# Performance work log

Hardware: AMD Instinct MI355X
Metric: run time of the kernel (lower is better)

Reference implementation:

```python
import jax, jax.numpy as jnp
import numpy as np

NL = 4   # numLayers (modules are shared across layers)
H = 8    # numSignalHeads; contextAttention has embed_dim=1 with 1 head


def _ln(x, g, b, eps=1e-10):
    m = x.mean(-1, keepdims=True)
    v = ((x - m) ** 2).mean(-1, keepdims=True)
    return (x - m) / jnp.sqrt(v + eps) * g + b


def _forward(signalData, contextualData, Ws, bs, bn_g, bn_b,
             cWq, cWk, cWv, cbq, cbk, cbv, cbias_k, cbias_v, cWo, cbo,
             xWq, xWk, xWv, xbq, xbk, xbv, xbias_k, xbias_v, xWo, xbo,
             W1, b1, W2, b2, W3, b3,
             ln_ff_g, ln_ff_b, ln_cas_g, ln_cas_b, ln_fin_g, ln_fin_b):
    B, S, E = signalData.shape
    dh = E // H
    scale = float(1.0 / np.sqrt(dh))
    # synthesizeContext: Linear(C,18) + BatchNorm1d(18, track_running_stats=False -> batch stats)
    ec = contextualData @ Ws.T + bs                       # (B,18)
    mu = ec.mean(0)
    var = ((ec - mu) ** 2).mean(0)                        # biased var (PyTorch BN)
    ec = (ec - mu) / jnp.sqrt(var + 1e-5) * bn_g + bn_b
    ec = ec[:, :, None]                                   # (B,18,1)
    sig = signalData
    for _ in range(NL):
        # --- self-attention on context: embed_dim=1, 1 head (head_dim=1, scale=1), add_bias_kv ---
        q = ec @ cWq.T + cbq                              # (B,18,1)
        k = jnp.concatenate([ec @ cWk.T + cbk, jnp.broadcast_to(cbias_k, (B, 1, 1))], axis=1)
        v = jnp.concatenate([ec @ cWv.T + cbv, jnp.broadcast_to(cbias_v, (B, 1, 1))], axis=1)
        a = jax.nn.softmax(jnp.einsum('bqd,bkd->bqk', q, k), axis=-1)
        sa = jnp.einsum('bqk,bkd->bqd', a, v) @ cWo.T + cbo
        ec = ec + sa
        # --- cross-attention: query/value = LN(signal) (E), key = context (kdim=1), add_bias_kv ---
        ns = _ln(sig, ln_cas_g, ln_cas_b)
        q = (ns @ xWq.T + xbq).reshape(B, S, H, dh)
        k = jnp.concatenate([ec @ xWk.T + xbk, jnp.broadcast_to(xbias_k, (B, 1, E))], axis=1).reshape(B, S + 1, H, dh)
        v = jnp.concatenate([ns @ xWv.T + xbv, jnp.broadcast_to(xbias_v, (B, 1, E))], axis=1).reshape(B, S + 1, H, dh)
        a = jax.nn.softmax(jnp.einsum('bqhd,bkhd->bhqk', q, k) * scale, axis=-1)
        ca = jnp.einsum('bhqk,bkhd->bqhd', a, v).reshape(B, S, E) @ xWo.T + xbo
        sig = sig + ca
        # --- feed-forward: Linear->SiLU->Linear->SiLU->Linear->SiLU (dropout = identity in eval) ---
        nf = _ln(sig, ln_ff_g, ln_ff_b)
        ff = jax.nn.silu(jax.nn.silu(jax.nn.silu(nf @ W1.T + b1) @ W2.T + b2) @ W3.T + b3)
        sig = sig + ff
    return _ln(sig, ln_fin_g, ln_fin_b)


def setup_inputs() -> dict:
    key = jax.random.key(0)
    ks = iter(jax.random.split(key, 48))
    r = lambda *s: jax.random.normal(next(ks), s, dtype=jnp.float32) * 0.05
    B, S, E, C = 4096, 18, 256, 512
    return dict(
        signalData=jax.random.normal(next(ks), (B, S, E), dtype=jnp.float32),
        contextualData=jax.random.normal(next(ks), (B, C), dtype=jnp.float32),
        Ws=r(18, C), bs=r(18), bn_g=jnp.ones(18, jnp.float32), bn_b=jnp.zeros(18, jnp.float32),
        cWq=r(1, 1), cWk=r(1, 1), cWv=r(1, 1), cbq=r(1), cbk=r(1), cbv=r(1),
        cbias_k=r(1), cbias_v=r(1), cWo=r(1, 1), cbo=r(1),
        xWq=r(E, E), xWk=r(E, 1), xWv=r(E, E), xbq=r(E), xbk=r(E), xbv=r(E),
        xbias_k=r(E), xbias_v=r(E), xWo=r(E, E), xbo=r(E),
        W1=r(32, E), b1=r(32), W2=r(16, 32), b2=r(16), W3=r(E, 16), b3=r(E),
        ln_ff_g=jnp.ones(E, jnp.float32), ln_ff_b=jnp.zeros(E, jnp.float32),
        ln_cas_g=jnp.ones(E, jnp.float32), ln_cas_b=jnp.zeros(E, jnp.float32),
        ln_fin_g=jnp.ones(E, jnp.float32), ln_fin_b=jnp.zeros(E, jnp.float32),
    )


def reference(signalData, contextualData, Ws, bs, bn_g, bn_b,
              cWq, cWk, cWv, cbq, cbk, cbv, cbias_k, cbias_v, cWo, cbo,
              xWq, xWk, xWv, xbq, xbk, xbv, xbias_k, xbias_v, xWo, xbo,
              W1, b1, W2, b2, W3, b3,
              ln_ff_g, ln_ff_b, ln_cas_g, ln_cas_b, ln_fin_g, ln_fin_b):
    return _forward(signalData, contextualData, Ws, bs, bn_g, bn_b,
                    cWq, cWk, cWv, cbq, cbk, cbv, cbias_k, cbias_v, cWo, cbo,
                    xWq, xWk, xWv, xbq, xbk, xbv, xbias_k, xbias_v, xWo, xbo,
                    W1, b1, W2, b2, W3, b3,
                    ln_ff_g, ln_ff_b, ln_cas_g, ln_cas_b, ln_fin_g, ln_fin_b)
```

## Files before the change

kernel.cpp:

```cpp
#include <hip/hip_runtime.h>

typedef unsigned short u16;
typedef __attribute__((ext_vector_type(8))) short bf16x8;
typedef __attribute__((ext_vector_type(4))) float f32x4;
typedef __attribute__((ext_vector_type(4))) unsigned int u32x4;
typedef __attribute__((ext_vector_type(2))) unsigned int u32x2;

#define MROWS 18
#define MT 2
#define SWZ(r,c)  ((c) ^ (((r)&7)<<3))
#define SWZV(n,j) ((j) ^ (((n)&3)<<3))
#define SWZP(i,j) ((j) ^ (((i)&3)<<3))

__device__ inline u16 f2bf(float f){
  unsigned int u = __float_as_uint(f);
  return (u16)((u + 0x7fffu + ((u>>16)&1u)) >> 16);
}
__device__ inline unsigned int packbf(float a, float b){
  return (unsigned int)f2bf(a) | ((unsigned int)f2bf(b)<<16);
}
__device__ inline float bfloat_lo(unsigned int u){ return __uint_as_float(u<<16); }
__device__ inline float bfloat_hi(unsigned int u){ return __uint_as_float(u & 0xffff0000u); }
__device__ inline float bf2f(u16 h){ return __uint_as_float(((unsigned int)h)<<16); }
__device__ inline float wred(float v){
  #pragma unroll
  for (int m=1;m<64;m<<=1) v += __shfl_xor(v, m, 64);
  return v;
}
__device__ inline float silu_f(float x){ return x / (1.f + __expf(-x)); }
__device__ inline f32x4 mfma16(bf16x8 a, bf16x8 b, f32x4 c){
  return __builtin_amdgcn_mfma_f32_16x16x32_bf16(a, b, c, 0, 0, 0);
}

struct Params {
  const float *sigIn;
  const float *bn_g, *bn_b;
  const float *cWq,*cWk,*cWv,*cbq,*cbk,*cbv,*cbias_k,*cbias_v,*cWo,*cbo;
  const float *xbv, *xbias_v, *xbo;
  const float *b1,*b2,*b3;
  const float *g_cas,*b_cas,*g_ff,*b_ff,*g_fin,*b_fin;
  const u16 *Wv,*Wo,*Wq3,*W1b,*W2b,*W3p;
  const float *bias3, *ecr_t, *mu, *rstd;
  float *out;
};

__global__ void k_prep(const float* __restrict__ xWq, const float* __restrict__ xWk,
                       const float* __restrict__ xWv, const float* __restrict__ xWo,
                       const float* __restrict__ xbq, const float* __restrict__ xbk,
                       const float* __restrict__ xbias_k,
                       const float* __restrict__ W1, const float* __restrict__ W2,
                       const float* __restrict__ W3,
                       u16* Wv, u16* Wo, u16* Wq3, u16* W1b, u16* W2b, u16* W3p, float* bias3){
  const int gid = blockIdx.x*blockDim.x + threadIdx.x;
  const int gsz = gridDim.x*blockDim.x;
  for (int i=gid;i<65536;i+=gsz) Wv[i]=f2bf(xWv[i]);
  for (int i=gid;i<65536;i+=gsz) Wo[i]=f2bf(xWo[i]);
  for (int i=gid;i<8192;i+=gsz)  W1b[i]=f2bf(W1[i]);
  for (int i=gid;i<512;i+=gsz)   W2b[i]=f2bf(W2[i]);
  for (int i=gid;i<8192;i+=gsz){ int o=i>>5, k=i&31; W3p[i] = (k<16)? f2bf(W3[o*16+k]) : (u16)0; }
  for (int i=gid;i<8192;i+=gsz){
    int r=i>>8, c=i&255;
    u16 outv = 0;
    if (r<24){
      int h=r&7, sel=r>>3;
      const float* vec = sel==0? xWk : (sel==1? xbk : xbias_k);
      float s=0.f;
      for (int d=0;d<32;++d) s += xWq[(size_t)(h*32+d)*256+c]*vec[h*32+d];
      outv = f2bf(s);
    }
    Wq3[i]=outv;
  }
  for (int i=gid;i<24;i+=gsz){
    int h=i&7, sel=i>>3;
    const float* vec = sel==0? xWk : (sel==1? xbk : xbias_k);
    float s=0.f; for (int d=0;d<32;++d) s += xbq[h*32+d]*vec[h*32+d];
    bias3[i]=s;
  }
}

__global__ void k_ec(const float* __restrict__ ctx, const float* __restrict__ Ws,
                     const float* __restrict__ bs, float* __restrict__ ecr_t){
  const int wave = threadIdx.x>>6, lane = threadIdx.x&63;
  const int b = blockIdx.x*4 + wave;
  const float* c = ctx + (size_t)b*512 + lane*8;
  const float4 a0 = *(const float4*)c, a1 = *(const float4*)(c+4);
  float cv[8] = {a0.x,a0.y,a0.z,a0.w,a1.x,a1.y,a1.z,a1.w};
  #pragma unroll 1
  for (int j=0;j<18;++j){
    const float* w = Ws + j*512 + lane*8;
    const float4 w0 = *(const float4*)w, w1 = *(const float4*)(w+4);
    float s = cv[0]*w0.x + cv[1]*w0.y + cv[2]*w0.z + cv[3]*w0.w
            + cv[4]*w1.x + cv[5]*w1.y + cv[6]*w1.z + cv[7]*w1.w;
    s = wred(s);
    if (lane==0) ecr_t[(size_t)j*4096 + b] = s + bs[j];
  }
}

__global__ void k_bn(const float* __restrict__ ecr_t, float* __restrict__ mu, float* __restrict__ rstd){
  __shared__ float red[256];
  const int j = blockIdx.x, tid = threadIdx.x;
  float s=0.f, s2=0.f;
  for (int b=tid;b<4096;b+=256){ float v = ecr_t[(size_t)j*4096+b]; s+=v; s2+=v*v; }
  red[tid]=s; __syncthreads();
  for (int o=128;o>0;o>>=1){ if(tid<o) red[tid]+=red[tid+o]; __syncthreads(); }
  float S = red[0]; __syncthreads();
  red[tid]=s2; __syncthreads();
  for (int o=128;o>0;o>>=1){ if(tid<o) red[tid]+=red[tid+o]; __syncthreads(); }
  float S2 = red[0];
  if (tid==0){ float m = S*(1.f/4096.f); float v = S2*(1.f/4096.f) - m*m;
               mu[j]=m; rstd[j]=rsqrtf(v+1e-5f); }
}

__global__ __launch_bounds__(256, 2) void k_main(Params P){
  __shared__ __attribute__((aligned(16))) u16 s_sig[MROWS][256];
  __shared__ __attribute__((aligned(16))) u16 s_ns [MROWS][256];
  __shared__ __attribute__((aligned(16))) u16 s_vT [256][32];
  __shared__ __attribute__((aligned(16))) u16 s_p  [8][MROWS][32];
  __shared__ __attribute__((aligned(16))) u16 s_h1 [MROWS][32];
  __shared__ float s_qq[MROWS][24];
  __shared__ float s_ec[MROWS];
  __shared__ float s_inv[8][MROWS];

  const int tid  = threadIdx.x;
  const int wave = tid >> 6;
  const int lane = tid & 63;
  const int lr   = lane & 15;
  const int lkg  = lane >> 4;
  const int kof  = lkg * 8;
  const int dr   = lkg * 4;
  const int b0   = blockIdx.x;

  for (int idx = tid*8; idx < MROWS*256; idx += 256*8){
    const int row = idx >> 8, col = idx & 255;
    const float* src = P.sigIn + (size_t)b0*18*256 + idx;
    const float4 a = *(const float4*)src;
    const float4 b = *(const float4*)(src+4);
    u32x4 w;
    w[0]=packbf(a.x,a.y); w[1]=packbf(a.z,a.w);
    w[2]=packbf(b.x,b.y); w[3]=packbf(b.z,b.w);
    *(u32x4*)&s_sig[row][SWZ(row,col)] = w;
  }
  {
    const int n = tid;
    s_vT[n][SWZV(n,19)] = 0;
    #pragma unroll
    for (int jp=10; jp<16; ++jp) *(unsigned int*)&s_vT[n][SWZV(n,2*jp)] = 0u;
    s_vT[n][SWZV(n,18)] = f2bf(P.xbias_v[n]);
  }
  if (lane < 36){
    const int h = 2*wave + (lane>=18 ? 1:0);
    const int i = lane - (lane>=18 ? 18:0);
    #pragma unroll
    for (int jp=10; jp<16; ++jp) *(unsigned int*)&s_p[h][i][SWZP(i,2*jp)] = 0u;
  }
  if (tid < MROWS){
    const float raw = P.ecr_t[(size_t)tid*4096 + b0];
    s_ec[tid] = (raw - P.mu[tid]) * P.rstd[tid] * P.bn_g[tid] + P.bn_b[tid];
  }
  __syncthreads();

  auto ln_rows = [&](const float* g, const float* bvec, int wbase, int wstep){
    for (int r = wbase; r < MROWS; r += wstep){
      const int col = lane*4;
      const u32x2 raw = *(const u32x2*)&s_sig[r][SWZ(r,col)];
      const float x0 = bfloat_lo(raw[0]), x1 = bfloat_hi(raw[0]);
      const float x2 = bfloat_lo(raw[1]), x3 = bfloat_hi(raw[1]);
      const float m = wred(x0+x1+x2+x3)*(1.f/256.f);
      const float d0=x0-m, d1=x1-m, d2=x2-m, d3=x3-m;
      const float rs = rsqrtf(wred(d0*d0+d1*d1+d2*d2+d3*d3)*(1.f/256.f)+1e-10f);
      const float4 gv = *(const float4*)(g+col);
      const float4 bv = *(const float4*)(bvec+col);
      u32x2 o;
      o[0] = packbf(d0*rs*gv.x+bv.x, d1*rs*gv.y+bv.y);
      o[1] = packbf(d2*rs*gv.z+bv.z, d3*rs*gv.w+bv.w);
      *(u32x2*)&s_ns[r][SWZ(r,col)] = o;
    }
  };

  for (int layer = 0; layer < 4; ++layer){
    if (wave == 0){
      if (lane < MROWS){
        const int i = lane;
        const float cwq=P.cWq[0], cbq=P.cbq[0], cwk=P.cWk[0], cbk=P.cbk[0];
        const float cwv=P.cWv[0], cbv=P.cbv[0], ck1=P.cbias_k[0], cv1=P.cbias_v[0];
        const float cwo=P.cWo[0], cbo=P.cbo[0];
        const float qi = s_ec[i]*cwq + cbq;
        float mx = qi*ck1;
        #pragma unroll
        for (int j=0;j<18;++j) mx = fmaxf(mx, qi*(s_ec[j]*cwk + cbk));
        float den=0.f, o=0.f;
        #pragma unroll
        for (int j=0;j<18;++j){
          const float pp=__expf(qi*(s_ec[j]*cwk + cbk)-mx);
          den+=pp; o+=pp*(s_ec[j]*cwv+cbv);
        }
        const float pp=__expf(qi*ck1-mx); den+=pp; o+=pp*cv1;
        s_ec[i] = s_ec[i] + (o/den)*cwo + cbo;
      }
    } else {
      ln_rows(P.g_cas, P.b_cas, wave-1, 3);
    }
    __syncthreads();

    {
      f32x4 accV[MT][4]; f32x4 accQ[MT];
      #pragma unroll
      for (int mt=0;mt<MT;++mt){
        accQ[mt] = f32x4{0.f,0.f,0.f,0.f};
        #pragma unroll
        for (int nt=0;nt<4;++nt) accV[mt][nt] = f32x4{0.f,0.f,0.f,0.f};
      }
      for (int kk=0; kk<8; ++kk){
        const int k0 = kk*32 + kof;
        bf16x8 afr[MT];
        #pragma unroll
        for (int mt=0;mt<MT;++mt){
          const int row = mt*16 + lr;
          u32x4 raw = u32x4{0u,0u,0u,0u};
          if (row < MROWS) raw = *(const u32x4*)&s_ns[row][SWZ(row,k0)];
          afr[mt] = __builtin_bit_cast(bf16x8, raw);
        }
        #pragma unroll
        for (int nt=0;nt<4;++nt){
          const int n = (wave*4+nt)*16 + lr;
          const bf16x8 bfr = __builtin_bit_cast(bf16x8, *(const u32x4*)(P.Wv + (size_t)n*256 + k0));
          #pragma unroll
          for (int mt=0;mt<MT;++mt) accV[mt][nt] = mfma16(afr[mt], bfr, accV[mt][nt]);
        }
        if (wave < 2){
          const bf16x8 bq = __builtin_bit_cast(bf16x8, *(const u32x4*)(P.Wq3 + (size_t)(wave*16+lr)*256 + k0));
          #pragma unroll
          for (int mt=0;mt<MT;++mt) accQ[mt] = mfma16(afr[mt], bq, accQ[mt]);
        }
      }
      #pragma unroll
      for (int nt=0;nt<4;++nt){
        const int n = (wave*4+nt)*16 + lr;
        const float bias = P.xbv[n];
        #pragma unroll
        for (int mt=0;mt<MT;++mt){
          const int c0 = mt*16 + dr;
          if (c0 + 3 < MROWS){
            u32x2 w;
            w[0] = packbf(accV[mt][nt][0]+bias, accV[mt][nt][1]+bias);
            w[1] = packbf(accV[mt][nt][2]+bias, accV[mt][nt][3]+bias);
            *(u32x2*)&s_vT[n][SWZV(n,c0)] = w;
          } else if (c0 < MROWS){
            #pragma unroll
            for (int q=0;q<2;++q) s_vT[n][SWZV(n,c0+q)] = f2bf(accV[mt][nt][q]+bias);
          }
        }
      }
      if (wave < 2){
        const int c = wave*16 + lr;
        if (c < 24){
          const float bias = P.bias3[c];
          #pragma unroll
          for (int mt=0;mt<MT;++mt){
            #pragma unroll
            for (int q=0;q<4;++q){
              const int row = mt*16 + dr + q;
              if (row < MROWS) s_qq[row][c] = accQ[mt][q] + bias;
            }
          }
        }
      }
    }
    __syncthreads();

    if (lane < 36){
      const int h = 2*wave + (lane>=18 ? 1:0);
      const int i = lane - (lane>=18 ? 18:0);
      const float scale = 0.17677669529663687f;
      const float qw = s_qq[i][h]*scale, qb = s_qq[i][8+h]*scale, s18 = s_qq[i][16+h]*scale;
      float mx = s18;
      #pragma unroll
      for (int j=0;j<18;++j) mx = fmaxf(mx, qw*s_ec[j] + qb);
      float den = 0.f;
      #pragma unroll
      for (int jj=0;jj<9;++jj){
        const float p0 = __expf(qw*s_ec[2*jj]   + qb - mx);
        const float p1 = __expf(qw*s_ec[2*jj+1] + qb - mx);
        den += p0 + p1;
        *(unsigned int*)&s_p[h][i][SWZP(i,2*jj)] = packbf(p0, p1);
      }
      const float p18 = __expf(s18 - mx); den += p18;
      *(unsigned int*)&s_p[h][i][SWZP(i,18)] = packbf(p18, 0.f);
      s_inv[h][i] = 1.f/den;
    }

    #pragma unroll
    for (int hb=0; hb<2; ++hb){
      const int h = wave*2 + hb;
      const bf16x8 a0 = __builtin_bit_cast(bf16x8, *(const u32x4*)&s_p[h][lr][SWZP(lr,kof)]);
      u32x4 zr = u32x4{0u,0u,0u,0u};
      if (lr < 2) zr = *(const u32x4*)&s_p[h][16+lr][SWZP(16+lr,kof)];
      const bf16x8 a1 = __builtin_bit_cast(bf16x8, zr);
      f32x4 d[MT][2];
      #pragma unroll
      for (int nt=0;nt<2;++nt){
        const int vn = h*32 + nt*16 + lr;
        const bf16x8 b = __builtin_bit_cast(bf16x8, *(const u32x4*)&s_vT[vn][SWZV(vn,kof)]);
        d[0][nt] = mfma16(a0, b, f32x4{0.f,0.f,0.f,0.f});
        d[1][nt] = mfma16(a1, b, f32x4{0.f,0.f,0.f,0.f});
      }
      #pragma unroll
      for (int nt=0;nt<2;++nt){
        #pragma unroll
        for (int mt=0;mt<MT;++mt){
          #pragma unroll
          for (int q=0;q<4;++q){
            const int row = mt*16 + dr + q;
            if (row < MROWS){
              s_ns[row][SWZ(row, h*32 + nt*16 + lr)] = f2bf(d[mt][nt][q]*s_inv[h][row]);
            }
          }
        }
      }
    }
    __syncthreads();

    {
      f32x4 acc[MT][4];
      #pragma unroll
      for (int mt=0;mt<MT;++mt){
        #pragma unroll
        for (int nt=0;nt<4;++nt) acc[mt][nt] = f32x4{0.f,0.f,0.f,0.f};
      }
      for (int kk=0; kk<8; ++kk){
        const int k0 = kk*32 + kof;
        bf16x8 afr[MT];
        #pragma unroll
        for (int mt=0;mt<MT;++mt){
          const int row = mt*16 + lr;
          u32x4 raw = u32x4{0u,0u,0u,0u};
          if (row < MROWS) raw = *(const u32x4*)&s_ns[row][SWZ(row,k0)];
          afr[mt] = __builtin_bit_cast(bf16x8, raw);
        }
        #pragma unroll
        for (int nt=0;nt<4;++nt){
          const int n = (wave*4+nt)*16 + lr;
          const bf16x8 bfr = __builtin_bit_cast(bf16x8, *(const u32x4*)(P.Wo + (size_t)n*256 + k0));
          #pragma unroll
          for (int mt=0;mt<MT;++mt) acc[mt][nt] = mfma16(afr[mt], bfr, acc[mt][nt]);
        }
      }
      #pragma unroll
      for (int nt=0;nt<4;++nt){
        const int n = (wave*4+nt)*16 + lr;
        const float bias = P.xbo[n];
        #pragma unroll
        for (int mt=0;mt<MT;++mt){
          #pragma unroll
          for (int q=0;q<4;++q){
            const int row = mt*16 + dr + q;
            if (row < MROWS){
              const int si = SWZ(row,n);
              s_sig[row][si] = f2bf(bf2f(s_sig[row][si]) + acc[mt][nt][q] + bias);
            }
          }
        }
      }
    }
    __syncthreads();

    ln_rows(P.g_ff, P.b_ff, wave, 4);
    __syncthreads();

    if (wave < 2){
      f32x4 acc[2];
      acc[0] = f32x4{0.f,0.f,0.f,0.f}; acc[1] = f32x4{0.f,0.f,0.f,0.f};
      for (int kk=0; kk<8; ++kk){
        const int k0 = kk*32 + kof;
        const int row = wave*16 + lr;
        u32x4 raw = u32x4{0u,0u,0u,0u};
        if (row < MROWS) raw = *(const u32x4*)&s_ns[row][SWZ(row,k0)];
        const bf16x8 afr = __builtin_bit_cast(bf16x8, raw);
        #pragma unroll
        for (int nt=0;nt<2;++nt){
          const bf16x8 bfr = __builtin_bit_cast(bf16x8, *(const u32x4*)(P.W1b + (size_t)(nt*16+lr)*256 + k0));
          acc[nt] = mfma16(afr, bfr, acc[nt]);
        }
      }
      #pragma unroll
      for (int nt=0;nt<2;++nt){
        const int c = nt*16 + lr;
        const float bias = P.b1[c];
        #pragma unroll
        for (int q=0;q<4;++q){
          const int row = wave*16 + dr + q;
          if (row < MROWS) s_h1[row][c] = f2bf(silu_f(acc[nt][q] + bias));
        }
      }
      {
        const int row_a = wave*16 + lr;
        u32x4 raw = u32x4{0u,0u,0u,0u};
        if (row_a < MROWS) raw = *(const u32x4*)&s_h1[row_a][kof];
        const bf16x8 a = __builtin_bit_cast(bf16x8, raw);
        const bf16x8 b = __builtin_bit_cast(bf16x8, *(const u32x4*)(P.W2b + (size_t)lr*32 + kof));
        f32x4 acc2 = mfma16(a, b, f32x4{0.f,0.f,0.f,0.f});
        const float bias = P.b2[lr];
        #pragma unroll
        for (int q=0;q<4;++q){
          const int row = wave*16 + dr + q;
          if (row < MROWS){
            s_h1[row][lr]    = f2bf(silu_f(acc2[q] + bias));
            s_h1[row][lr+16] = 0;
          }
        }
      }
    }
    __syncthreads();

    {
      bf16x8 afr[MT];
      #pragma unroll
      for (int mt=0;mt<MT;++mt){
        const int row = mt*16 + lr;
        u32x4 raw = u32x4{0u,0u,0u,0u};
        if (row < MROWS) raw = *(const u32x4*)&s_h1[row][kof];
        afr[mt] = __builtin_bit_cast(bf16x8, raw);
      }
      f32x4 acc[MT][4];
      #pragma unroll
      for (int nt=0;nt<4;++nt){
        const int n = (wave*4+nt)*16 + lr;
        const bf16x8 bfr = __builtin_bit_cast(bf16x8, *(const u32x4*)(P.W3p + (size_t)n*32 + kof));
        #pragma unroll
        for (int mt=0;mt<MT;++mt) acc[mt][nt] = mfma16(afr[mt], bfr, f32x4{0.f,0.f,0.f,0.f});
      }
      #pragma unroll
      for (int nt=0;nt<4;++nt){
        const int n = (wave*4+nt)*16 + lr;
        const float b3v = P.b3[n];
        #pragma unroll
        for (int mt=0;mt<MT;++mt){
          #pragma unroll
          for (int q=0;q<4;++q){
            const int row = mt*16 + dr + q;
            if (row < MROWS){
              const int si = SWZ(row,n);
              s_sig[row][si] = f2bf(bf2f(s_sig[row][si]) + silu_f(acc[mt][nt][q] + b3v));
            }
          }
        }
      }
    }
    __syncthreads();
  }

  {
    for (int r = wave; r < MROWS; r += 4){
      const int col = lane*4;
      const u32x2 raw = *(const u32x2*)&s_sig[r][SWZ(r,col)];
      const float x0 = bfloat_lo(raw[0]), x1 = bfloat_hi(raw[0]);
      const float x2 = bfloat_lo(raw[1]), x3 = bfloat_hi(raw[1]);
      const float m = wred(x0+x1+x2+x3)*(1.f/256.f);
      const float d0=x0-m, d1=x1-m, d2=x2-m, d3=x3-m;
      const float rs = rsqrtf(wred(d0*d0+d1*d1+d2*d2+d3*d3)*(1.f/256.f)+1e-10f);
      const float4 gv = *(const float4*)(P.g_fin+col);
      const float4 bv = *(const float4*)(P.b_fin+col);
      float4 o;
      o.x = d0*rs*gv.x+bv.x; o.y = d1*rs*gv.y+bv.y;
      o.z = d2*rs*gv.z+bv.z; o.w = d3*rs*gv.w+bv.w;
      *(float4*)(P.out + ((size_t)b0*18 + r)*256 + col) = o;
    }
  }
}

extern "C" void kernel_launch(void* const* d_in, const int* in_sizes, int n_in,
                              void* d_out, int out_size, void* d_ws, size_t ws_size,
                              hipStream_t stream) {
  (void)in_sizes; (void)n_in; (void)out_size; (void)ws_size;
  const float* sigIn   = (const float*)d_in[0];
  const float* ctx     = (const float*)d_in[1];
  const float* Ws      = (const float*)d_in[2];
  const float* bs      = (const float*)d_in[3];
  const float* bn_g    = (const float*)d_in[4];
  const float* bn_b    = (const float*)d_in[5];
  const float* cWq     = (const float*)d_in[6];
  const float* cWk     = (const float*)d_in[7];
  const float* cWv     = (const float*)d_in[8];
  const float* cbq     = (const float*)d_in[9];
  const float* cbk     = (const float*)d_in[10];
  const float* cbv     = (const float*)d_in[11];
  const float* cbias_k = (const float*)d_in[12];
  const float* cbias_v = (const float*)d_in[13];
  const float* cWo     = (const float*)d_in[14];
  const float* cbo     = (const float*)d_in[15];
  const float* xWq     = (const float*)d_in[16];
  const float* xWk     = (const float*)d_in[17];
  const float* xWv     = (const float*)d_in[18];
  const float* xbq     = (const float*)d_in[19];
  const float* xbk     = (const float*)d_in[20];
  const float* xbv     = (const float*)d_in[21];
  const float* xbias_k = (const float*)d_in[22];
  const float* xbias_v = (const float*)d_in[23];
  const float* xWo     = (const float*)d_in[24];
  const float* xbo     = (const float*)d_in[25];
  const float* W1      = (const float*)d_in[26];
  const float* b1      = (const float*)d_in[27];
  const float* W2      = (const float*)d_in[28];
  const float* b2      = (const float*)d_in[29];
  const float* W3      = (const float*)d_in[30];
  const float* b3      = (const float*)d_in[31];
  const float* g_ff    = (const float*)d_in[32];
  const float* b_ff    = (const float*)d_in[33];
  const float* g_cas   = (const float*)d_in[34];
  const float* b_cas   = (const float*)d_in[35];
  const float* g_fin   = (const float*)d_in[36];
  const float* b_fin   = (const float*)d_in[37];

  char* ws = (char*)d_ws;
  u16*  Wv    = (u16*)(ws);
  u16*  Wo    = (u16*)(ws + 131072);
  u16*  Wq3   = (u16*)(ws + 262144);
  u16*  W1b   = (u16*)(ws + 278528);
  u16*  W2b   = (u16*)(ws + 294912);
  u16*  W3p   = (u16*)(ws + 295936);
  float* bias3= (float*)(ws + 312320);
  float* ecr_t= (float*)(ws + 312448);
  float* mu   = (float*)(ws + 607360);
  float* rstd = (float*)(ws + 607488);

  k_prep<<<dim3(64), dim3(256), 0, stream>>>(xWq, xWk, xWv, xWo, xbq, xbk, xbias_k,
                                             W1, W2, W3, Wv, Wo, Wq3, W1b, W2b, W3p, bias3);
  k_ec<<<dim3(1024), dim3(256), 0, stream>>>(ctx, Ws, bs, ecr_t);
  k_bn<<<dim3(18), dim3(256), 0, stream>>>(ecr_t, mu, rstd);

  Params P;
  P.sigIn = sigIn; P.bn_g = bn_g; P.bn_b = bn_b;
  P.cWq=cWq; P.cWk=cWk; P.cWv=cWv; P.cbq=cbq; P.cbk=cbk; P.cbv=cbv;
  P.cbias_k=cbias_k; P.cbias_v=cbias_v; P.cWo=cWo; P.cbo=cbo;
  P.xbv=xbv; P.xbias_v=xbias_v; P.xbo=xbo;
  P.b1=b1; P.b2=b2; P.b3=b3;
  P.g_cas=g_cas; P.b_cas=b_cas; P.g_ff=g_ff; P.b_ff=b_ff; P.g_fin=g_fin; P.b_fin=b_fin;
  P.Wv=Wv; P.Wo=Wo; P.Wq3=Wq3; P.W1b=W1b; P.W2b=W2b; P.W3p=W3p;
  P.bias3=bias3; P.ecr_t=ecr_t; P.mu=mu; P.rstd=rstd;
  P.out = (float*)d_out;

  k_main<<<dim3(4096), dim3(256), 0, stream>>>(P);
}
```

Baseline: 1.060 ms.

## Double block to 512 threads and build attention probabilities in registers

Raises the main kernel to 8 waves per block and redistributes the GEMM tiles so each wave handles half as many output columns. The cross-attention now gives one head per wave and computes the softmax max and denominator per row. It then recomputes the normalized probabilities directly into MFMA A-fragments, removing the shared-memory probability buffer and its zero-init. This buys more parallelism per batch element and removes the LDS round-trip, at the cost of recomputing exponentials and a higher launch-bounds occupancy target that may pressure registers.

```diff
diff --git a/kernel.cpp b/kernel.cpp
--- a/kernel.cpp
+++ b/kernel.cpp
@@ -10,7 +10,6 @@
 #define MT 2
 #define SWZ(r,c)  ((c) ^ (((r)&7)<<3))
 #define SWZV(n,j) ((j) ^ (((n)&3)<<3))
-#define SWZP(i,j) ((j) ^ (((i)&3)<<3))
 
 __device__ inline u16 f2bf(float f){
   unsigned int u = __float_as_uint(f);
@@ -111,14 +110,14 @@
                mu[j]=m; rstd[j]=rsqrtf(v+1e-5f); }
 }
 
-__global__ __launch_bounds__(256, 2) void k_main(Params P){
+__global__ __launch_bounds__(512, 4) void k_main(Params P){
   __shared__ __attribute__((aligned(16))) u16 s_sig[MROWS][256];
   __shared__ __attribute__((aligned(16))) u16 s_ns [MROWS][256];
   __shared__ __attribute__((aligned(16))) u16 s_vT [256][32];
-  __shared__ __attribute__((aligned(16))) u16 s_p  [8][MROWS][32];
   __shared__ __attribute__((aligned(16))) u16 s_h1 [MROWS][32];
-  __shared__ float s_qq[MROWS][24];
+  __shared__ float s_qq[MROWS][28];
   __shared__ float s_ec[MROWS];
+  __shared__ float s_mx [8][MROWS];
   __shared__ float s_inv[8][MROWS];
 
   const int tid  = threadIdx.x;
@@ -129,8 +128,9 @@
   const int kof  = lkg * 8;
   const int dr   = lkg * 4;
   const int b0   = blockIdx.x;
-
-  for (int idx = tid*8; idx < MROWS*256; idx += 256*8){
+  const float scale = 0.17677669529663687f;
+
+  for (int idx = tid*8; idx < MROWS*256; idx += 512*8){
     const int row = idx >> 8, col = idx & 255;
     const float* src = P.sigIn + (size_t)b0*18*256 + idx;
     const float4 a = *(const float4*)src;
@@ -140,18 +140,12 @@
     w[2]=packbf(b.x,b.y); w[3]=packbf(b.z,b.w);
     *(u32x4*)&s_sig[row][SWZ(row,col)] = w;
   }
-  {
+  if (tid < 256){
     const int n = tid;
     s_vT[n][SWZV(n,19)] = 0;
     #pragma unroll
     for (int jp=10; jp<16; ++jp) *(unsigned int*)&s_vT[n][SWZV(n,2*jp)] = 0u;
     s_vT[n][SWZV(n,18)] = f2bf(P.xbias_v[n]);
-  }
-  if (lane < 36){
-    const int h = 2*wave + (lane>=18 ? 1:0);
-    const int i = lane - (lane>=18 ? 18:0);
-    #pragma unroll
-    for (int jp=10; jp<16; ++jp) *(unsigned int*)&s_p[h][i][SWZP(i,2*jp)] = 0u;
   }
   if (tid < MROWS){
     const float raw = P.ecr_t[(size_t)tid*4096 + b0];
@@ -198,18 +192,15 @@
         s_ec[i] = s_ec[i] + (o/den)*cwo + cbo;
       }
     } else {
-      ln_rows(P.g_cas, P.b_cas, wave-1, 3);
+      ln_rows(P.g_cas, P.b_cas, wave-1, 7);
     }
     __syncthreads();
 
     {
-      f32x4 accV[MT][4]; f32x4 accQ[MT];
-      #pragma unroll
-      for (int mt=0;mt<MT;++mt){
-        accQ[mt] = f32x4{0.f,0.f,0.f,0.f};
-        #pragma unroll
-        for (int nt=0;nt<4;++nt) accV[mt][nt] = f32x4{0.f,0.f,0.f,0.f};
-      }
+      f32x4 acc[2][MT]; f32x4 accQ[MT];
+      #pragma unroll
+      for (int j=0;j<2;++j){ acc[j][0]=f32x4{0,0,0,0}; acc[j][1]=f32x4{0,0,0,0}; }
+      accQ[0]=f32x4{0,0,0,0}; accQ[1]=f32x4{0,0,0,0};
       for (int kk=0; kk<8; ++kk){
         const int k0 = kk*32 + kof;
         bf16x8 afr[MT];
@@ -221,11 +212,11 @@
           afr[mt] = __builtin_bit_cast(bf16x8, raw);
         }
         #pragma unroll
-        for (int nt=0;nt<4;++nt){
-          const int n = (wave*4+nt)*16 + lr;
+        for (int j=0;j<2;++j){
+          const int n = (j*8+wave)*16 + lr;
           const bf16x8 bfr = __builtin_bit_cast(bf16x8, *(const u32x4*)(P.Wv + (size_t)n*256 + k0));
           #pragma unroll
-          for (int mt=0;mt<MT;++mt) accV[mt][nt] = mfma16(afr[mt], bfr, accV[mt][nt]);
+          for (int mt=0;mt<MT;++mt) acc[j][mt] = mfma16(afr[mt], bfr, acc[j][mt]);
         }
         if (wave < 2){
           const bf16x8 bq = __builtin_bit_cast(bf16x8, *(const u32x4*)(P.Wq3 + (size_t)(wave*16+lr)*256 + k0));
@@ -234,21 +225,18 @@
         }
       }
       #pragma unroll
-      for (int nt=0;nt<4;++nt){
-        const int n = (wave*4+nt)*16 + lr;
+      for (int j=0;j<2;++j){
+        const int n = (j*8+wave)*16 + lr;
         const float bias = P.xbv[n];
-        #pragma unroll
-        for (int mt=0;mt<MT;++mt){
-          const int c0 = mt*16 + dr;
-          if (c0 + 3 < MROWS){
-            u32x2 w;
-            w[0] = packbf(accV[mt][nt][0]+bias, accV[mt][nt][1]+bias);
-            w[1] = packbf(accV[mt][nt][2]+bias, accV[mt][nt][3]+bias);
-            *(u32x2*)&s_vT[n][SWZV(n,c0)] = w;
-          } else if (c0 < MROWS){
-            #pragma unroll
-            for (int q=0;q<2;++q) s_vT[n][SWZV(n,c0+q)] = f2bf(accV[mt][nt][q]+bias);
-          }
+        {
+          u32x2 w;
+          w[0] = packbf(acc[j][0][0]+bias, acc[j][0][1]+bias);
+          w[1] = packbf(acc[j][0][2]+bias, acc[j][0][3]+bias);
+          *(u32x2*)&s_vT[n][SWZV(n,dr)] = w;
+        }
+        if (dr == 0){
+          s_vT[n][SWZV(n,16)] = f2bf(acc[j][1][0]+bias);
+          s_vT[n][SWZV(n,17)] = f2bf(acc[j][1][1]+bias);
         }
       }
       if (wave < 2){
@@ -268,52 +256,72 @@
     }
     __syncthreads();
 
-    if (lane < 36){
-      const int h = 2*wave + (lane>=18 ? 1:0);
-      const int i = lane - (lane>=18 ? 18:0);
-      const float scale = 0.17677669529663687f;
-      const float qw = s_qq[i][h]*scale, qb = s_qq[i][8+h]*scale, s18 = s_qq[i][16+h]*scale;
-      float mx = s18;
-      #pragma unroll
-      for (int j=0;j<18;++j) mx = fmaxf(mx, qw*s_ec[j] + qb);
-      float den = 0.f;
-      #pragma unroll
-      for (int jj=0;jj<9;++jj){
-        const float p0 = __expf(qw*s_ec[2*jj]   + qb - mx);
-        const float p1 = __expf(qw*s_ec[2*jj+1] + qb - mx);
-        den += p0 + p1;
-        *(unsigned int*)&s_p[h][i][SWZP(i,2*jj)] = packbf(p0, p1);
-      }
-      const float p18 = __expf(s18 - mx); den += p18;
-      *(unsigned int*)&s_p[h][i][SWZP(i,18)] = packbf(p18, 0.f);
-      s_inv[h][i] = 1.f/den;
-    }
-
-    #pragma unroll
-    for (int hb=0; hb<2; ++hb){
-      const int h = wave*2 + hb;
-      const bf16x8 a0 = __builtin_bit_cast(bf16x8, *(const u32x4*)&s_p[h][lr][SWZP(lr,kof)]);
-      u32x4 zr = u32x4{0u,0u,0u,0u};
-      if (lr < 2) zr = *(const u32x4*)&s_p[h][16+lr][SWZP(16+lr,kof)];
-      const bf16x8 a1 = __builtin_bit_cast(bf16x8, zr);
-      f32x4 d[MT][2];
+    {
+      const int h = wave;
+      if (lane < MROWS){
+        const int i = lane;
+        const float qw = s_qq[i][h]*scale, qb = s_qq[i][8+h]*scale, s18 = s_qq[i][16+h]*scale;
+        float mx = s18;
+        #pragma unroll
+        for (int j=0;j<18;++j) mx = fmaxf(mx, qw*s_ec[j] + qb);
+        float den = __expf(s18-mx);
+        #pragma unroll
+        for (int j=0;j<18;++j) den += __expf(qw*s_ec[j] + qb - mx);
+        s_mx[h][i]  = mx;
+        s_inv[h][i] = 1.f/den;
+      }
+      bf16x8 a0, a1;
+      {
+        const float qw = s_qq[lr][h]*scale, qb = s_qq[lr][8+h]*scale, s18 = s_qq[lr][16+h]*scale;
+        const float mx = s_mx[h][lr], inv = s_inv[h][lr];
+        u16 pa[8];
+        #pragma unroll
+        for (int e=0;e<8;++e){
+          const int k = kof + e;
+          const float ecv = s_ec[k<18 ? k : 0];
+          float pv = (k<18) ? __expf(qw*ecv+qb-mx) : ((k==18) ? __expf(s18-mx) : 0.f);
+          pa[e] = f2bf(pv*inv);
+        }
+        u32x4 w; 
+        w[0]=(unsigned)pa[0]|((unsigned)pa[1]<<16); w[1]=(unsigned)pa[2]|((unsigned)pa[3]<<16);
+        w[2]=(unsigned)pa[4]|((unsigned)pa[5]<<16); w[3]=(unsigned)pa[6]|((unsigned)pa[7]<<16);
+        a0 = __builtin_bit_cast(bf16x8, w);
+      }
+      {
+        u32x4 w = u32x4{0u,0u,0u,0u};
+        if (lr < 2){
+          const int rI = 16+lr;
+          const float qw = s_qq[rI][h]*scale, qb = s_qq[rI][8+h]*scale, s18 = s_qq[rI][16+h]*scale;
+          const float mx = s_mx[h][rI], inv = s_inv[h][rI];
+          u16 pa[8];
+          #pragma unroll
+          for (int e=0;e<8;++e){
+            const int k = kof + e;
+            const float ecv = s_ec[k<18 ? k : 0];
+            float pv = (k<18) ? __expf(qw*ecv+qb-mx) : ((k==18) ? __expf(s18-mx) : 0.f);
+            pa[e] = f2bf(pv*inv);
+          }
+          w[0]=(unsigned)pa[0]|((unsigned)pa[1]<<16); w[1]=(unsigned)pa[2]|((unsigned)pa[3]<<16);
+          w[2]=(unsigned)pa[4]|((unsigned)pa[5]<<16); w[3]=(unsigned)pa[6]|((unsigned)pa[7]<<16);
+        }
+        a1 = __builtin_bit_cast(bf16x8, w);
+      }
       #pragma unroll
       for (int nt=0;nt<2;++nt){
         const int vn = h*32 + nt*16 + lr;
         const bf16x8 b = __builtin_bit_cast(bf16x8, *(const u32x4*)&s_vT[vn][SWZV(vn,kof)]);
-        d[0][nt] = mfma16(a0, b, f32x4{0.f,0.f,0.f,0.f});
-        d[1][nt] = mfma16(a1, b, f32x4{0.f,0.f,0.f,0.f});
-      }
-      #pragma unroll
-      for (int nt=0;nt<2;++nt){
-        #pragma unroll
-        for (int mt=0;mt<MT;++mt){
-          #pragma unroll
-          for (int q=0;q<4;++q){
-            const int row = mt*16 + dr + q;
-            if (row < MROWS){
-              s_ns[row][SWZ(row, h*32 + nt*16 + lr)] = f2bf(d[mt][nt][q]*s_inv[h][row]);
-            }
+        const f32x4 d0 = mfma16(a0, b, f32x4{0,0,0,0});
+        const f32x4 d1 = mfma16(a1, b, f32x4{0,0,0,0});
+        #pragma unroll
+        for (int q=0;q<4;++q){
+          const int row = dr + q;
+          s_ns[row][SWZ(row, h*32 + nt*16 + lr)] = f2bf(d0[q]);
+        }
+        if (dr == 0){
+          #pragma unroll
+          for (int q=0;q<2;++q){
+            const int row = 16 + q;
+            s_ns[row][SWZ(row, h*32 + nt*16 + lr)] = f2bf(d1[q]);
           }
         }
       }
@@ -321,12 +329,9 @@
     __syncthreads();
 
     {
-      f32x4 acc[MT][4];
-      #pragma unroll
-      for (int mt=0;mt<MT;++mt){
-        #pragma unroll
-        for (int nt=0;nt<4;++nt) acc[mt][nt] = f32x4{0.f,0.f,0.f,0.f};
-      }
+      f32x4 acc[2][MT];
+      #pragma unroll
+      for (int j=0;j<2;++j){ acc[j][0]=f32x4{0,0,0,0}; acc[j][1]=f32x4{0,0,0,0}; }
       for (int kk=0; kk<8; ++kk){
         const int k0 = kk*32 + kof;
         bf16x8 afr[MT];
@@ -338,16 +343,16 @@
           afr[mt] = __builtin_bit_cast(bf16x8, raw);
         }
         #pragma unroll
-        for (int nt=0;nt<4;++nt){
-          const int n = (wave*4+nt)*16 + lr;
+        for (int nt=0;nt<2;++nt){
+          const int n = (wave*2+nt)*16 + lr;
           const bf16x8 bfr = __builtin_bit_cast(bf16x8, *(const u32x4*)(P.Wo + (size_t)n*256 + k0));
           #pragma unroll
-          for (int mt=0;mt<MT;++mt) acc[mt][nt] = mfma16(afr[mt], bfr, acc[mt][nt]);
-        }
-      }
-      #pragma unroll
-      for (int nt=0;nt<4;++nt){
-        const int n = (wave*4+nt)*16 + lr;
+          for (int mt=0;mt<MT;++mt) acc[nt][mt] = mfma16(afr[mt], bfr, acc[nt][mt]);
+        }
+      }
+      #pragma unroll
+      for (int nt=0;nt<2;++nt){
+        const int n = (wave*2+nt)*16 + lr;
         const float bias = P.xbo[n];
         #pragma unroll
         for (int mt=0;mt<MT;++mt){
@@ -356,7 +361,7 @@
             const int row = mt*16 + dr + q;
             if (row < MROWS){
               const int si = SWZ(row,n);
-              s_sig[row][si] = f2bf(bf2f(s_sig[row][si]) + acc[mt][nt][q] + bias);
+              s_sig[row][si] = f2bf(bf2f(s_sig[row][si]) + acc[nt][mt][q] + bias);
             }
           }
         }
@@ -364,12 +369,12 @@
     }
     __syncthreads();
 
-    ln_rows(P.g_ff, P.b_ff, wave, 4);
+    ln_rows(P.g_ff, P.b_ff, wave, 8);
     __syncthreads();
 
     if (wave < 2){
       f32x4 acc[2];
-      acc[0] = f32x4{0.f,0.f,0.f,0.f}; acc[1] = f32x4{0.f,0.f,0.f,0.f};
+      acc[0]=f32x4{0,0,0,0}; acc[1]=f32x4{0,0,0,0};
       for (int kk=0; kk<8; ++kk){
         const int k0 = kk*32 + kof;
         const int row = wave*16 + lr;
@@ -398,7 +403,7 @@
         if (row_a < MROWS) raw = *(const u32x4*)&s_h1[row_a][kof];
         const bf16x8 a = __builtin_bit_cast(bf16x8, raw);
         const bf16x8 b = __builtin_bit_cast(bf16x8, *(const u32x4*)(P.W2b + (size_t)lr*32 + kof));
-        f32x4 acc2 = mfma16(a, b, f32x4{0.f,0.f,0.f,0.f});
+        f32x4 acc2 = mfma16(a, b, f32x4{0,0,0,0});
         const float bias = P.b2[lr];
         #pragma unroll
         for (int q=0;q<4;++q){
@@ -421,26 +426,20 @@
         if (row < MROWS) raw = *(const u32x4*)&s_h1[row][kof];
         afr[mt] = __builtin_bit_cast(bf16x8, raw);
       }
-      f32x4 acc[MT][4];
-      #pragma unroll
-      for (int nt=0;nt<4;++nt){
-        const int n = (wave*4+nt)*16 + lr;
+      #pragma unroll
+      for (int nt=0;nt<2;++nt){
+        const int n = (wave*2+nt)*16 + lr;
         const bf16x8 bfr = __builtin_bit_cast(bf16x8, *(const u32x4*)(P.W3p + (size_t)n*32 + kof));
-        #pragma unroll
-        for (int mt=0;mt<MT;++mt) acc[mt][nt] = mfma16(afr[mt], bfr, f32x4{0.f,0.f,0.f,0.f});
-      }
-      #pragma unroll
-      for (int nt=0;nt<4;++nt){
-        const int n = (wave*4+nt)*16 + lr;
         const float b3v = P.b3[n];
         #pragma unroll
         for (int mt=0;mt<MT;++mt){
+          const f32x4 acc = mfma16(afr[mt], bfr, f32x4{0,0,0,0});
           #pragma unroll
           for (int q=0;q<4;++q){
             const int row = mt*16 + dr + q;
             if (row < MROWS){
               const int si = SWZ(row,n);
-              s_sig[row][si] = f2bf(bf2f(s_sig[row][si]) + silu_f(acc[mt][nt][q] + b3v));
+              s_sig[row][si] = f2bf(bf2f(s_sig[row][si]) + silu_f(acc[q] + b3v));
             }
           }
         }
@@ -450,7 +449,7 @@
   }
 
   {
-    for (int r = wave; r < MROWS; r += 4){
+    for (int r = wave; r < MROWS; r += 8){
       const int col = lane*4;
       const u32x2 raw = *(const u32x2*)&s_sig[r][SWZ(r,col)];
       const float x0 = bfloat_lo(raw[0]), x1 = bfloat_hi(raw[0]);
@@ -539,5 +538,5 @@
   P.bias3=bias3; P.ecr_t=ecr_t; P.mu=mu; P.rstd=rstd;
   P.out = (float*)d_out;
 
-  k_main<<<dim3(4096), dim3(256), 0, stream>>>(P);
-}
+  k_main<<<dim3(4096), dim3(512), 0, stream>>>(P);
+}
```

Measured after the change: 1.281 ms. +20.8%, slower.
